# Kernel tuning notes

Hardware: AMD Instinct MI355X
Metric: run time of the kernel (lower is better)

Reference implementation:

```python
import jax, jax.numpy as jnp
import numpy as np

N_TOKEN = 64
H = 16
D = 1024
D_K = 64
D_V = 64
S3 = 30  # 3 * S, number of gated leading positions
GATE_INIT = 10.0


def setup_inputs() -> dict:
    key = jax.random.key(0)
    ks = jax.random.split(key, 8)
    B, L = 32, 2048
    x = jax.random.normal(ks[0], (B, L, D), dtype=jnp.float32)
    q_init = (1.0 / D_K) ** 0.5
    q_tok = jax.random.uniform(ks[1], (1, N_TOKEN, D), minval=-q_init, maxval=q_init, dtype=jnp.float32)
    scale = 0.02
    Wq = jax.random.normal(ks[2], (D, H * D_K), dtype=jnp.float32) * scale
    Wk = jax.random.normal(ks[3], (D, H * D_K), dtype=jnp.float32) * scale
    Wv = jax.random.normal(ks[4], (D, H * D_V), dtype=jnp.float32) * scale
    Wfc = jax.random.normal(ks[5], (H * D_V, D), dtype=jnp.float32) * scale
    gate_logit = -jnp.ones((S3,), dtype=jnp.float32) * GATE_INIT  # matches module init
    gamma = jnp.ones((D,), dtype=jnp.float32)
    beta = jnp.zeros((D,), dtype=jnp.float32)
    return {"x": x, "q_tok": q_tok, "Wq": Wq, "Wk": Wk, "Wv": Wv, "Wfc": Wfc,
            "gate_logit": gate_logit, "gamma": gamma, "beta": beta}


def reference(x, q_tok, Wq, Wk, Wv, Wfc, gate_logit, gamma, beta):
    # x: [B, L, D]; q_tok: [1, n_token, D]. Dropout is identity (eval mode).
    B, L, _ = x.shape
    temp = D_K ** 0.5

    # Cumulative-product gate over the first 30 positions (the torch for-loop).
    gate = jnp.cumprod(1.0 - jax.nn.sigmoid(gate_logit))  # [30]
    x1 = x.at[:, :S3].multiply(gate[None, :, None])

    q = (q_tok @ Wq).reshape(N_TOKEN, H, D_K)          # [n, H, dk]
    k = (x @ Wk).reshape(B, L, H, D_K)                  # [B, L, H, dk]
    v = (x1 @ Wv).reshape(B, L, H, D_V)                 # [B, L, H, dv]

    scores = jnp.einsum('nhd,blhd->bhnl', q / temp, k)  # [B, H, n, L]
    attn = jax.nn.softmax(scores, axis=-1)
    out = jnp.einsum('bhnl,blhd->bnhd', attn, v).reshape(B, N_TOKEN, H * D_V)

    out = out @ Wfc + q_tok                              # residual with query tokens

    # LayerNorm over last dim, eps=1e-6
    mu = jnp.mean(out, axis=-1, keepdims=True)
    var = jnp.mean(jnp.square(out - mu), axis=-1, keepdims=True)
    out = (out - mu) * jax.lax.rsqrt(var + 1e-6) * gamma + beta
    return out
```

## Files before the change

kernel.cpp:

```cpp
#include <hip/hip_runtime.h>
#include <stdint.h>

typedef unsigned short u16;
typedef short bf16x8 __attribute__((ext_vector_type(8)));
typedef float f32x4 __attribute__((ext_vector_type(4)));

__device__ __forceinline__ u16 f2b(float f) {
  uint32_t u = __builtin_bit_cast(uint32_t, f);
  u += 0x7fffu + ((u >> 16) & 1u);
  return (u16)(u >> 16);
}

__device__ __forceinline__ void gload_lds16(const void* g, void* l) {
  __builtin_amdgcn_global_load_lds(
      (const __attribute__((address_space(1))) void*)g,
      (__attribute__((address_space(3))) void*)l, 16, 0, 0);
}

__global__ void gate_kernel(const float* __restrict__ gl, float* __restrict__ gate) {
  if (threadIdx.x == 0 && blockIdx.x == 0) {
    float g = 1.0f;
    for (int i = 0; i < 30; ++i) {
      float s = 1.0f / (1.0f + __expf(-gl[i]));
      g *= (1.0f - s);
      gate[i] = g;
    }
  }
}

__global__ __launch_bounds__(256) void cvt_x_kernel(const float* __restrict__ x,
                                                    u16* __restrict__ xb) {
  int64_t i = ((int64_t)blockIdx.x * 256 + threadIdx.x) * 8;
  float4 a = *(const float4*)(x + i);
  float4 b = *(const float4*)(x + i + 4);
  union { u16 u[8]; bf16x8 v; } o;
  o.u[0] = f2b(a.x); o.u[1] = f2b(a.y); o.u[2] = f2b(a.z); o.u[3] = f2b(a.w);
  o.u[4] = f2b(b.x); o.u[5] = f2b(b.y); o.u[6] = f2b(b.z); o.u[7] = f2b(b.w);
  *(bf16x8*)(xb + i) = o.v;
}

__global__ __launch_bounds__(256) void transpose_w_kernel(const float* __restrict__ src,
                                                          u16* __restrict__ dst) {
  __shared__ float ls[64][65];
  int t = threadIdx.x;
  int bx = blockIdx.x & 15;
  int by = blockIdx.x >> 4;
  int r0 = by * 64, c0 = bx * 64;
  int tr = t >> 6, tc = t & 63;
#pragma unroll
  for (int i = 0; i < 16; ++i)
    ls[tr + i * 4][tc] = src[(int64_t)(r0 + tr + i * 4) * 1024 + c0 + tc];
  __syncthreads();
#pragma unroll
  for (int i = 0; i < 16; ++i)
    dst[(int64_t)(c0 + tr + i * 4) * 1024 + r0 + tc] = f2b(ls[tc][tr + i * 4]);
}

__global__ __launch_bounds__(256) void q_kernel(const float* __restrict__ q_tok,
                                                const float* __restrict__ Wq,
                                                u16* __restrict__ qb) {
  __shared__ float Qs[64][65];
  __shared__ float Ws[64][65];
  int h = blockIdx.x;
  int t = threadIdx.x;
  int tn = t >> 4, tk = t & 15;
  float acc[4][4] = {};
  for (int dt = 0; dt < 16; ++dt) {
    __syncthreads();
#pragma unroll
    for (int i = 0; i < 16; ++i) {
      int idx = t + i * 256;
      int rr = idx >> 6, cc = idx & 63;
      Qs[rr][cc] = q_tok[rr * 1024 + dt * 64 + cc];
      Ws[rr][cc] = Wq[(dt * 64 + rr) * 1024 + h * 64 + cc];
    }
    __syncthreads();
    for (int d = 0; d < 64; ++d) {
      float qv[4], wv[4];
#pragma unroll
      for (int i = 0; i < 4; ++i) qv[i] = Qs[tn * 4 + i][d];
#pragma unroll
      for (int j = 0; j < 4; ++j) wv[j] = Ws[d][tk * 4 + j];
#pragma unroll
      for (int i = 0; i < 4; ++i)
#pragma unroll
        for (int j = 0; j < 4; ++j) acc[i][j] += qv[i] * wv[j];
    }
  }
  const float sc = 1.44269504f / 8.0f;
#pragma unroll
  for (int i = 0; i < 4; ++i)
#pragma unroll
    for (int j = 0; j < 4; ++j)
      qb[(h * 64 + tn * 4 + i) * 64 + tk * 4 + j] = f2b(acc[i][j] * sc);
}

__global__ __launch_bounds__(256) void kv_gemm_kernel(
    const u16* __restrict__ xb, const u16* __restrict__ wkvT,
    const float* __restrict__ gate, u16* __restrict__ kbuf, u16* __restrict__ vT) {
  __shared__ u16 As[4096];
  __shared__ u16 Bs[4096];
  int bid = blockIdx.x;
  int mb = bid >> 4, nb = bid & 15;
  int m0 = mb * 128, n0 = nb * 128;
  int t = threadIdx.x, w = t >> 6, lane = t & 63;
  int wm = (w >> 1) * 64, wn = (w & 1) * 64;
  bool isV = (n0 >= 1024);
  f32x4 acc[4][4] = {};
  int srow = w * 32 + (lane >> 2);
  int scol = (lane & 3) * 8;
  const u16* aSrc = xb + (int64_t)(m0 + srow) * 1024 + scol;
  const u16* bSrc = wkvT + (int64_t)(n0 + srow) * 1024 + scol;
  u16* aDst = As + w * 1024;
  u16* bDst = Bs + w * 1024;
  for (int kt = 0; kt < 32; ++kt) {
    __syncthreads();
    int ko = kt * 32;
    gload_lds16(aSrc + ko, aDst);
    gload_lds16(aSrc + 16 * 1024 + ko, aDst + 512);
    gload_lds16(bSrc + ko, bDst);
    gload_lds16(bSrc + 16 * 1024 + ko, bDst + 512);
    __syncthreads();
    int l15 = lane & 15, lh = (lane >> 4) * 8;
    bf16x8 af[4], bf[4];
#pragma unroll
    for (int i = 0; i < 4; ++i) af[i] = *(const bf16x8*)(As + (wm + i * 16 + l15) * 32 + lh);
#pragma unroll
    for (int j = 0; j < 4; ++j) bf[j] = *(const bf16x8*)(Bs + (wn + j * 16 + l15) * 32 + lh);
    if (!isV) {
#pragma unroll
      for (int i = 0; i < 4; ++i)
#pragma unroll
        for (int j = 0; j < 4; ++j)
          acc[i][j] = __builtin_amdgcn_mfma_f32_16x16x32_bf16(af[i], bf[j], acc[i][j], 0, 0, 0);
    } else {
#pragma unroll
      for (int i = 0; i < 4; ++i)
#pragma unroll
        for (int j = 0; j < 4; ++j)
          acc[i][j] = __builtin_amdgcn_mfma_f32_16x16x32_bf16(bf[i], af[j], acc[i][j], 0, 0, 0);
    }
  }
  int b = m0 >> 11, lbase = m0 & 2047;
  int l15 = lane & 15, lr = (lane >> 4) * 4;
  if (!isV) {
#pragma unroll
    for (int i = 0; i < 4; ++i)
#pragma unroll
      for (int j = 0; j < 4; ++j) {
        int gcol = n0 + wn + j * 16 + l15;
        int h = gcol >> 6, dk = gcol & 63;
#pragma unroll
        for (int r = 0; r < 4; ++r) {
          int l = lbase + wm + i * 16 + lr + r;
          kbuf[(int64_t)((b * 16 + h) * 2048 + l) * 64 + dk] = f2b(acc[i][j][r]);
        }
      }
  } else {
#pragma unroll
    for (int j = 0; j < 4; ++j) {
      int lloc = wm + j * 16 + l15;
      int l = lbase + lloc;
      float g = 1.0f;
      if (lbase == 0 && lloc < 30) g = gate[lloc];
#pragma unroll
      for (int i = 0; i < 4; ++i) {
#pragma unroll
        for (int r = 0; r < 4; ++r) {
          int gn = (n0 - 1024) + wn + i * 16 + lr + r;
          int h = gn >> 6, dv = gn & 63;
          vT[(int64_t)((b * 16 + h) * 64 + dv) * 2048 + l] = f2b(acc[i][j][r] * g);
        }
      }
    }
  }
}

__global__ __launch_bounds__(256) void attn_kernel(
    const u16* __restrict__ qb, const u16* __restrict__ kbuf,
    const u16* __restrict__ vT, u16* __restrict__ attnout) {
  __shared__ u16 Ps[4096];
  int bid = blockIdx.x;
  int b = bid >> 4, h = bid & 15;
  int t = threadIdx.x, w = t >> 6, lane = t & 63;
  int l15 = lane & 15, lh8 = (lane >> 4) * 8;
  bf16x8 qf0 = *(const bf16x8*)(qb + (h * 64 + w * 16 + l15) * 64 + lh8);
  bf16x8 qf1 = *(const bf16x8*)(qb + (h * 64 + w * 16 + l15) * 64 + 32 + lh8);
  const u16* kB = kbuf + (int64_t)(b * 16 + h) * (2048 * 64);
  const u16* vB = vT + (int64_t)(b * 16 + h) * (64 * 2048);
  char* PsW = (char*)Ps + w * 2048;
  float m_r[4] = {-1e30f, -1e30f, -1e30f, -1e30f};
  float s_r[4] = {0.f, 0.f, 0.f, 0.f};
  f32x4 O[4] = {};
  for (int lt = 0; lt < 32; ++lt) {
    int l0 = lt * 64;
    f32x4 S[4];
#pragma unroll
    for (int ls = 0; ls < 4; ++ls) {
      const u16* kr = kB + (l0 + ls * 16 + l15) * 64 + lh8;
      bf16x8 k0 = *(const bf16x8*)(kr);
      bf16x8 k1 = *(const bf16x8*)(kr + 32);
      f32x4 s = {};
      s = __builtin_amdgcn_mfma_f32_16x16x32_bf16(qf0, k0, s, 0, 0, 0);
      s = __builtin_amdgcn_mfma_f32_16x16x32_bf16(qf1, k1, s, 0, 0, 0);
      S[ls] = s;
    }
    float scale[4];
#pragma unroll
    for (int r = 0; r < 4; ++r) {
      float tm = fmaxf(fmaxf(S[0][r], S[1][r]), fmaxf(S[2][r], S[3][r]));
#pragma unroll
      for (int msk = 1; msk < 16; msk <<= 1)
        tm = fmaxf(tm, __shfl_xor(tm, msk, 16));
      float mn = fmaxf(m_r[r], tm);
      scale[r] = exp2f(m_r[r] - mn);
      m_r[r] = mn;
    }
#pragma unroll
    for (int ls = 0; ls < 4; ++ls)
#pragma unroll
      for (int r = 0; r < 4; ++r) S[ls][r] = exp2f(S[ls][r] - m_r[r]);
#pragma unroll
    for (int r = 0; r < 4; ++r) {
      float ps = (S[0][r] + S[1][r]) + (S[2][r] + S[3][r]);
      s_r[r] = s_r[r] * scale[r] + ps;
    }
#pragma unroll
    for (int ls = 0; ls < 4; ++ls)
#pragma unroll
      for (int r = 0; r < 4; ++r) {
        int row = (lane >> 4) * 4 + r;
        int off = (ls * 16 + l15) * 2;
        *(u16*)(PsW + row * 128 + (off ^ ((row & 7) << 4))) = f2b(S[ls][r]);
      }
#pragma unroll
    for (int d = 0; d < 4; ++d)
#pragma unroll
      for (int r = 0; r < 4; ++r) O[d][r] *= scale[r];
    bf16x8 pa0, pa1;
    {
      int off0 = (lane >> 4) * 16;
      pa0 = *(const bf16x8*)(PsW + l15 * 128 + (off0 ^ ((l15 & 7) << 4)));
      pa1 = *(const bf16x8*)(PsW + l15 * 128 + ((off0 + 64) ^ ((l15 & 7) << 4)));
    }
#pragma unroll
    for (int d = 0; d < 4; ++d) {
      const u16* vr = vB + (d * 16 + l15) * 2048 + l0 + lh8;
      bf16x8 v0 = *(const bf16x8*)(vr);
      bf16x8 v1 = *(const bf16x8*)(vr + 32);
      O[d] = __builtin_amdgcn_mfma_f32_16x16x32_bf16(pa0, v0, O[d], 0, 0, 0);
      O[d] = __builtin_amdgcn_mfma_f32_16x16x32_bf16(pa1, v1, O[d], 0, 0, 0);
    }
  }
#pragma unroll
  for (int r = 0; r < 4; ++r) {
    float s = s_r[r];
#pragma unroll
    for (int msk = 1; msk < 16; msk <<= 1) s += __shfl_xor(s, msk, 16);
    float inv = 1.0f / s;
#pragma unroll
    for (int d = 0; d < 4; ++d) O[d][r] *= inv;
  }
#pragma unroll
  for (int d = 0; d < 4; ++d)
#pragma unroll
    for (int r = 0; r < 4; ++r) {
      int n = w * 16 + (lane >> 4) * 4 + r;
      attnout[(int64_t)(b * 64 + n) * 1024 + h * 64 + d * 16 + l15] = f2b(O[d][r]);
    }
}

__global__ __launch_bounds__(256) void fc_gemm_kernel(
    const u16* __restrict__ a, const u16* __restrict__ bT,
    const float* __restrict__ q_tok, float* __restrict__ out) {
  __shared__ u16 As[4096];
  __shared__ u16 Bs[4096];
  int bid = blockIdx.x;
  int mb = bid >> 3, nb = bid & 7;
  int m0 = mb * 128, n0 = nb * 128;
  int t = threadIdx.x, w = t >> 6, lane = t & 63;
  int wm = (w >> 1) * 64, wn = (w & 1) * 64;
  f32x4 acc[4][4] = {};
  int srow = w * 32 + (lane >> 2);
  int scol = (lane & 3) * 8;
  const u16* aSrc = a + (int64_t)(m0 + srow) * 1024 + scol;
  const u16* bSrc = bT + (int64_t)(n0 + srow) * 1024 + scol;
  u16* aDst = As + w * 1024;
  u16* bDst = Bs + w * 1024;
  for (int kt = 0; kt < 32; ++kt) {
    __syncthreads();
    int ko = kt * 32;
    gload_lds16(aSrc + ko, aDst);
    gload_lds16(aSrc + 16 * 1024 + ko, aDst + 512);
    gload_lds16(bSrc + ko, bDst);
    gload_lds16(bSrc + 16 * 1024 + ko, bDst + 512);
    __syncthreads();
    int l15 = lane & 15, lh = (lane >> 4) * 8;
    bf16x8 af[4], bf[4];
#pragma unroll
    for (int i = 0; i < 4; ++i) af[i] = *(const bf16x8*)(As + (wm + i * 16 + l15) * 32 + lh);
#pragma unroll
    for (int j = 0; j < 4; ++j) bf[j] = *(const bf16x8*)(Bs + (wn + j * 16 + l15) * 32 + lh);
#pragma unroll
    for (int i = 0; i < 4; ++i)
#pragma unroll
      for (int j = 0; j < 4; ++j)
        acc[i][j] = __builtin_amdgcn_mfma_f32_16x16x32_bf16(af[i], bf[j], acc[i][j], 0, 0, 0);
  }
  int l15 = lane & 15, lr = (lane >> 4) * 4;
#pragma unroll
  for (int i = 0; i < 4; ++i)
#pragma unroll
    for (int j = 0; j < 4; ++j) {
      int col = n0 + wn + j * 16 + l15;
#pragma unroll
      for (int r = 0; r < 4; ++r) {
        int row = m0 + wm + i * 16 + lr + r;
        out[(int64_t)row * 1024 + col] = acc[i][j][r] + q_tok[(row & 63) * 1024 + col];
      }
    }
}

__global__ __launch_bounds__(256) void ln_kernel(
    const float* __restrict__ fc, const float* __restrict__ gamma,
    const float* __restrict__ beta, float* __restrict__ out) {
  __shared__ float red[8];
  int row = blockIdx.x, t = threadIdx.x;
  float4 y = *(const float4*)(fc + (int64_t)row * 1024 + t * 4);
  float s = (y.x + y.y) + (y.z + y.w);
  float ss = (y.x * y.x + y.y * y.y) + (y.z * y.z + y.w * y.w);
#pragma unroll
  for (int msk = 1; msk < 64; msk <<= 1) {
    s += __shfl_xor(s, msk, 64);
    ss += __shfl_xor(ss, msk, 64);
  }
  if ((t & 63) == 0) { red[t >> 6] = s; red[4 + (t >> 6)] = ss; }
  __syncthreads();
  s = (red[0] + red[1]) + (red[2] + red[3]);
  ss = (red[4] + red[5]) + (red[6] + red[7]);
  float mu = s * (1.0f / 1024.0f);
  float var = ss * (1.0f / 1024.0f) - mu * mu;
  float rstd = rsqrtf(var + 1e-6f);
  float4 g = *(const float4*)(gamma + t * 4);
  float4 be = *(const float4*)(beta + t * 4);
  float4 o;
  o.x = (y.x - mu) * rstd * g.x + be.x;
  o.y = (y.y - mu) * rstd * g.y + be.y;
  o.z = (y.z - mu) * rstd * g.z + be.z;
  o.w = (y.w - mu) * rstd * g.w + be.w;
  *(float4*)(out + (int64_t)row * 1024 + t * 4) = o;
}

extern "C" void kernel_launch(void* const* d_in, const int* in_sizes, int n_in,
                              void* d_out, int out_size, void* d_ws, size_t ws_size,
                              hipStream_t stream) {
  const float* x     = (const float*)d_in[0];
  const float* q_tok = (const float*)d_in[1];
  const float* Wq    = (const float*)d_in[2];
  const float* Wk    = (const float*)d_in[3];
  const float* Wv    = (const float*)d_in[4];
  const float* Wfc   = (const float*)d_in[5];
  const float* gl    = (const float*)d_in[6];
  const float* gamma = (const float*)d_in[7];
  const float* beta  = (const float*)d_in[8];
  float* out = (float*)d_out;
  char* ws = (char*)d_ws;

  u16*   xb      = (u16*)(ws);
  u16*   kbuf    = (u16*)(ws + 134217728);
  u16*   vT      = (u16*)(ws + 268435456);
  u16*   wkvT    = (u16*)(ws + 402653184);
  u16*   wfcT    = (u16*)(ws + 406847488);
  u16*   qb      = (u16*)(ws + 408944640);
  float* gate    = (float*)(ws + 409075712);
  u16*   attnout = (u16*)(ws + 409076224);
  float* fcout   = (float*)(ws + 413270528);

  gate_kernel<<<1, 64, 0, stream>>>(gl, gate);
  cvt_x_kernel<<<32768, 256, 0, stream>>>(x, xb);
  transpose_w_kernel<<<256, 256, 0, stream>>>(Wk, wkvT);
  transpose_w_kernel<<<256, 256, 0, stream>>>(Wv, wkvT + 1024 * 1024);
  transpose_w_kernel<<<256, 256, 0, stream>>>(Wfc, wfcT);
  q_kernel<<<16, 256, 0, stream>>>(q_tok, Wq, qb);
  kv_gemm_kernel<<<8192, 256, 0, stream>>>(xb, wkvT, gate, kbuf, vT);
  attn_kernel<<<512, 256, 0, stream>>>(qb, kbuf, vT, attnout);
  fc_gemm_kernel<<<128, 256, 0, stream>>>(attnout, wfcT, q_tok, fcout);
  ln_kernel<<<2048, 256, 0, stream>>>(fcout, gamma, beta, out);
}
```

Before: 800.4 us.

## Rework GEMMs with swizzled K=64 LDS tiles, split-K attention, and MFMA q projection

The KV, FC and new Q GEMMs load 64-wide K tiles into XOR-swizzled LDS, which halves the number of barriers and avoids bank conflicts. Epilogues write vectorised 64-bit and float4 stores, and the KV GEMM block order is remapped for L2 locality. Attention is split four ways along L into 2048 blocks and followed by a separate combine kernel, which raises occupancy. The q projection becomes a bf16 MFMA GEMM. In exchange this adds extra launches and partial-result traffic, and the partials reuse the xb workspace region after it is consumed.

```diff
diff --git a/kernel.cpp b/kernel.cpp
--- a/kernel.cpp
+++ b/kernel.cpp
@@ -28,15 +28,15 @@
   }
 }
 
-__global__ __launch_bounds__(256) void cvt_x_kernel(const float* __restrict__ x,
-                                                    u16* __restrict__ xb) {
+__global__ __launch_bounds__(256) void cvt_kernel(const float* __restrict__ src,
+                                                  u16* __restrict__ dst) {
   int64_t i = ((int64_t)blockIdx.x * 256 + threadIdx.x) * 8;
-  float4 a = *(const float4*)(x + i);
-  float4 b = *(const float4*)(x + i + 4);
+  float4 a = *(const float4*)(src + i);
+  float4 b = *(const float4*)(src + i + 4);
   union { u16 u[8]; bf16x8 v; } o;
   o.u[0] = f2b(a.x); o.u[1] = f2b(a.y); o.u[2] = f2b(a.z); o.u[3] = f2b(a.w);
   o.u[4] = f2b(b.x); o.u[5] = f2b(b.y); o.u[6] = f2b(b.z); o.u[7] = f2b(b.w);
-  *(bf16x8*)(xb + i) = o.v;
+  *(bf16x8*)(dst + i) = o.v;
 }
 
 __global__ __launch_bounds__(256) void transpose_w_kernel(const float* __restrict__ src,
@@ -56,121 +56,145 @@
     dst[(int64_t)(c0 + tr + i * 4) * 1024 + r0 + tc] = f2b(ls[tc][tr + i * 4]);
 }
 
-__global__ __launch_bounds__(256) void q_kernel(const float* __restrict__ q_tok,
-                                                const float* __restrict__ Wq,
-                                                u16* __restrict__ qb) {
-  __shared__ float Qs[64][65];
-  __shared__ float Ws[64][65];
-  int h = blockIdx.x;
-  int t = threadIdx.x;
-  int tn = t >> 4, tk = t & 15;
-  float acc[4][4] = {};
-  for (int dt = 0; dt < 16; ++dt) {
-    __syncthreads();
-#pragma unroll
-    for (int i = 0; i < 16; ++i) {
-      int idx = t + i * 256;
-      int rr = idx >> 6, cc = idx & 63;
-      Qs[rr][cc] = q_tok[rr * 1024 + dt * 64 + cc];
-      Ws[rr][cc] = Wq[(dt * 64 + rr) * 1024 + h * 64 + cc];
-    }
-    __syncthreads();
-    for (int d = 0; d < 64; ++d) {
-      float qv[4], wv[4];
-#pragma unroll
-      for (int i = 0; i < 4; ++i) qv[i] = Qs[tn * 4 + i][d];
-#pragma unroll
-      for (int j = 0; j < 4; ++j) wv[j] = Ws[d][tk * 4 + j];
-#pragma unroll
-      for (int i = 0; i < 4; ++i)
-#pragma unroll
-        for (int j = 0; j < 4; ++j) acc[i][j] += qv[i] * wv[j];
+__global__ __launch_bounds__(256, 4) void q_gemm_kernel(
+    const u16* __restrict__ qtokb, const u16* __restrict__ wqT, u16* __restrict__ qb) {
+  __shared__ u16 As[4096];
+  __shared__ u16 Bs[8192];
+  int n0 = blockIdx.x * 128;
+  int t = threadIdx.x, w = t >> 6, lane = t & 63;
+  int wn = w * 32;
+  f32x4 acc[2][4] = {};
+  int l3 = lane >> 3;
+  int colE = ((lane & 7) ^ l3) * 8;
+  const u16* aS = qtokb + (int64_t)(w * 16 + l3) * 1024 + colE;
+  const u16* bS = wqT + (int64_t)(n0 + w * 32 + l3) * 1024 + colE;
+  u16* aD = As + w * 1024;
+  u16* bD = Bs + w * 2048;
+  int l15 = lane & 15, g16 = lane >> 4;
+  for (int kt = 0; kt < 16; ++kt) {
+    int ko = kt * 64;
+    __syncthreads();
+    gload_lds16(aS + ko, aD);
+    gload_lds16(aS + ko + 8192, aD + 512);
+#pragma unroll
+    for (int g = 0; g < 4; ++g) gload_lds16(bS + ko + g * 8192, bD + g * 512);
+    __syncthreads();
+#pragma unroll
+    for (int kk = 0; kk < 2; ++kk) {
+      int sl = ((kk * 4 + g16) ^ (l15 & 7)) * 8;
+      bf16x8 af[4], bf[2];
+#pragma unroll
+      for (int j = 0; j < 4; ++j) af[j] = *(const bf16x8*)(As + (j * 16 + l15) * 64 + sl);
+#pragma unroll
+      for (int i = 0; i < 2; ++i) bf[i] = *(const bf16x8*)(Bs + (wn + i * 16 + l15) * 64 + sl);
+#pragma unroll
+      for (int i = 0; i < 2; ++i)
+#pragma unroll
+        for (int j = 0; j < 4; ++j)
+          acc[i][j] = __builtin_amdgcn_mfma_f32_16x16x32_bf16(bf[i], af[j], acc[i][j], 0, 0, 0);
     }
   }
   const float sc = 1.44269504f / 8.0f;
-#pragma unroll
-  for (int i = 0; i < 4; ++i)
-#pragma unroll
-    for (int j = 0; j < 4; ++j)
-      qb[(h * 64 + tn * 4 + i) * 64 + tk * 4 + j] = f2b(acc[i][j] * sc);
-}
-
-__global__ __launch_bounds__(256) void kv_gemm_kernel(
+  int lr = g16 * 4;
+#pragma unroll
+  for (int i = 0; i < 2; ++i) {
+    int colg = n0 + wn + i * 16 + lr;
+#pragma unroll
+    for (int j = 0; j < 4; ++j) {
+      int qrow = j * 16 + l15;
+      u16 p[4];
+#pragma unroll
+      for (int r = 0; r < 4; ++r) p[r] = f2b(acc[i][j][r] * sc);
+      *(uint64_t*)(qb + qrow * 1024 + colg) = *(uint64_t*)p;
+    }
+  }
+}
+
+__global__ __launch_bounds__(256, 4) void kv_gemm_kernel(
     const u16* __restrict__ xb, const u16* __restrict__ wkvT,
     const float* __restrict__ gate, u16* __restrict__ kbuf, u16* __restrict__ vT) {
-  __shared__ u16 As[4096];
-  __shared__ u16 Bs[4096];
-  int bid = blockIdx.x;
+  __shared__ u16 As[8192];
+  __shared__ u16 Bs[8192];
+  int bid0 = blockIdx.x;
+  int bid = (bid0 & 7) * 1024 + (bid0 >> 3);
   int mb = bid >> 4, nb = bid & 15;
   int m0 = mb * 128, n0 = nb * 128;
   int t = threadIdx.x, w = t >> 6, lane = t & 63;
   int wm = (w >> 1) * 64, wn = (w & 1) * 64;
   bool isV = (n0 >= 1024);
   f32x4 acc[4][4] = {};
-  int srow = w * 32 + (lane >> 2);
-  int scol = (lane & 3) * 8;
-  const u16* aSrc = xb + (int64_t)(m0 + srow) * 1024 + scol;
-  const u16* bSrc = wkvT + (int64_t)(n0 + srow) * 1024 + scol;
-  u16* aDst = As + w * 1024;
-  u16* bDst = Bs + w * 1024;
-  for (int kt = 0; kt < 32; ++kt) {
-    __syncthreads();
-    int ko = kt * 32;
-    gload_lds16(aSrc + ko, aDst);
-    gload_lds16(aSrc + 16 * 1024 + ko, aDst + 512);
-    gload_lds16(bSrc + ko, bDst);
-    gload_lds16(bSrc + 16 * 1024 + ko, bDst + 512);
-    __syncthreads();
-    int l15 = lane & 15, lh = (lane >> 4) * 8;
-    bf16x8 af[4], bf[4];
-#pragma unroll
-    for (int i = 0; i < 4; ++i) af[i] = *(const bf16x8*)(As + (wm + i * 16 + l15) * 32 + lh);
-#pragma unroll
-    for (int j = 0; j < 4; ++j) bf[j] = *(const bf16x8*)(Bs + (wn + j * 16 + l15) * 32 + lh);
-    if (!isV) {
-#pragma unroll
-      for (int i = 0; i < 4; ++i)
-#pragma unroll
-        for (int j = 0; j < 4; ++j)
-          acc[i][j] = __builtin_amdgcn_mfma_f32_16x16x32_bf16(af[i], bf[j], acc[i][j], 0, 0, 0);
-    } else {
-#pragma unroll
-      for (int i = 0; i < 4; ++i)
-#pragma unroll
-        for (int j = 0; j < 4; ++j)
-          acc[i][j] = __builtin_amdgcn_mfma_f32_16x16x32_bf16(bf[i], af[j], acc[i][j], 0, 0, 0);
+  int l3 = lane >> 3;
+  int colE = ((lane & 7) ^ l3) * 8;
+  const u16* aS = xb + (int64_t)(m0 + w * 32 + l3) * 1024 + colE;
+  const u16* bS = wkvT + (int64_t)(n0 + w * 32 + l3) * 1024 + colE;
+  u16* aD = As + w * 2048;
+  u16* bD = Bs + w * 2048;
+  int l15 = lane & 15, g16 = lane >> 4;
+  for (int kt = 0; kt < 16; ++kt) {
+    int ko = kt * 64;
+    __syncthreads();
+#pragma unroll
+    for (int g = 0; g < 4; ++g) {
+      gload_lds16(aS + ko + g * 8192, aD + g * 512);
+      gload_lds16(bS + ko + g * 8192, bD + g * 512);
+    }
+    __syncthreads();
+#pragma unroll
+    for (int kk = 0; kk < 2; ++kk) {
+      int sl = ((kk * 4 + g16) ^ (l15 & 7)) * 8;
+      bf16x8 af[4], bf[4];
+#pragma unroll
+      for (int i = 0; i < 4; ++i) af[i] = *(const bf16x8*)(As + (wm + i * 16 + l15) * 64 + sl);
+#pragma unroll
+      for (int j = 0; j < 4; ++j) bf[j] = *(const bf16x8*)(Bs + (wn + j * 16 + l15) * 64 + sl);
+      if (!isV) {
+#pragma unroll
+        for (int i = 0; i < 4; ++i)
+#pragma unroll
+          for (int j = 0; j < 4; ++j)
+            acc[i][j] = __builtin_amdgcn_mfma_f32_16x16x32_bf16(bf[i], af[j], acc[i][j], 0, 0, 0);
+      } else {
+#pragma unroll
+        for (int i = 0; i < 4; ++i)
+#pragma unroll
+          for (int j = 0; j < 4; ++j)
+            acc[i][j] = __builtin_amdgcn_mfma_f32_16x16x32_bf16(af[i], bf[j], acc[i][j], 0, 0, 0);
+      }
     }
   }
   int b = m0 >> 11, lbase = m0 & 2047;
-  int l15 = lane & 15, lr = (lane >> 4) * 4;
+  int lr = g16 * 4;
   if (!isV) {
 #pragma unroll
-    for (int i = 0; i < 4; ++i)
+    for (int i = 0; i < 4; ++i) {
+      int dkg = n0 + wn + i * 16 + lr;
+      int h = dkg >> 6, dkk = dkg & 63;
 #pragma unroll
       for (int j = 0; j < 4; ++j) {
-        int gcol = n0 + wn + j * 16 + l15;
-        int h = gcol >> 6, dk = gcol & 63;
+        int l = lbase + wm + j * 16 + l15;
+        u16 p[4];
+#pragma unroll
+        for (int r = 0; r < 4; ++r) p[r] = f2b(acc[i][j][r]);
+        *(uint64_t*)(kbuf + ((int64_t)((b * 16 + h) * 2048 + l)) * 64 + dkk) = *(uint64_t*)p;
+      }
+    }
+  } else {
+#pragma unroll
+    for (int j = 0; j < 4; ++j) {
+      int dvg = (n0 - 1024) + wn + j * 16 + l15;
+      int h = dvg >> 6, dv = dvg & 63;
+#pragma unroll
+      for (int i = 0; i < 4; ++i) {
+        int lg = lbase + wm + i * 16 + lr;
+        u16 p[4];
 #pragma unroll
         for (int r = 0; r < 4; ++r) {
-          int l = lbase + wm + i * 16 + lr + r;
-          kbuf[(int64_t)((b * 16 + h) * 2048 + l) * 64 + dk] = f2b(acc[i][j][r]);
+          float val = acc[i][j][r];
+          int ll = lg + r;
+          if (ll < 30) val *= gate[ll];
+          p[r] = f2b(val);
         }
-      }
-  } else {
-#pragma unroll
-    for (int j = 0; j < 4; ++j) {
-      int lloc = wm + j * 16 + l15;
-      int l = lbase + lloc;
-      float g = 1.0f;
-      if (lbase == 0 && lloc < 30) g = gate[lloc];
-#pragma unroll
-      for (int i = 0; i < 4; ++i) {
-#pragma unroll
-        for (int r = 0; r < 4; ++r) {
-          int gn = (n0 - 1024) + wn + i * 16 + lr + r;
-          int h = gn >> 6, dv = gn & 63;
-          vT[(int64_t)((b * 16 + h) * 64 + dv) * 2048 + l] = f2b(acc[i][j][r] * g);
-        }
+        *(uint64_t*)(vT + ((int64_t)((b * 16 + h) * 64 + dv)) * 2048 + lg) = *(uint64_t*)p;
       }
     }
   }
@@ -178,22 +202,23 @@
 
 __global__ __launch_bounds__(256) void attn_kernel(
     const u16* __restrict__ qb, const u16* __restrict__ kbuf,
-    const u16* __restrict__ vT, u16* __restrict__ attnout) {
+    const u16* __restrict__ vT, float* __restrict__ pO,
+    float* __restrict__ pm, float* __restrict__ ps) {
   __shared__ u16 Ps[4096];
   int bid = blockIdx.x;
-  int b = bid >> 4, h = bid & 15;
+  int b = bid >> 6, h = (bid >> 2) & 15, c = bid & 3;
   int t = threadIdx.x, w = t >> 6, lane = t & 63;
-  int l15 = lane & 15, lh8 = (lane >> 4) * 8;
-  bf16x8 qf0 = *(const bf16x8*)(qb + (h * 64 + w * 16 + l15) * 64 + lh8);
-  bf16x8 qf1 = *(const bf16x8*)(qb + (h * 64 + w * 16 + l15) * 64 + 32 + lh8);
+  int l15 = lane & 15, g16 = lane >> 4, lh8 = g16 * 8;
+  bf16x8 qf0 = *(const bf16x8*)(qb + (w * 16 + l15) * 1024 + h * 64 + lh8);
+  bf16x8 qf1 = *(const bf16x8*)(qb + (w * 16 + l15) * 1024 + h * 64 + 32 + lh8);
   const u16* kB = kbuf + (int64_t)(b * 16 + h) * (2048 * 64);
   const u16* vB = vT + (int64_t)(b * 16 + h) * (64 * 2048);
   char* PsW = (char*)Ps + w * 2048;
   float m_r[4] = {-1e30f, -1e30f, -1e30f, -1e30f};
   float s_r[4] = {0.f, 0.f, 0.f, 0.f};
   f32x4 O[4] = {};
-  for (int lt = 0; lt < 32; ++lt) {
-    int l0 = lt * 64;
+  for (int lt = 0; lt < 8; ++lt) {
+    int l0 = c * 512 + lt * 64;
     f32x4 S[4];
 #pragma unroll
     for (int ls = 0; ls < 4; ++ls) {
@@ -222,14 +247,14 @@
       for (int r = 0; r < 4; ++r) S[ls][r] = exp2f(S[ls][r] - m_r[r]);
 #pragma unroll
     for (int r = 0; r < 4; ++r) {
-      float ps = (S[0][r] + S[1][r]) + (S[2][r] + S[3][r]);
-      s_r[r] = s_r[r] * scale[r] + ps;
+      float psm = (S[0][r] + S[1][r]) + (S[2][r] + S[3][r]);
+      s_r[r] = s_r[r] * scale[r] + psm;
     }
 #pragma unroll
     for (int ls = 0; ls < 4; ++ls)
 #pragma unroll
       for (int r = 0; r < 4; ++r) {
-        int row = (lane >> 4) * 4 + r;
+        int row = g16 * 4 + r;
         int off = (ls * 16 + l15) * 2;
         *(u16*)(PsW + row * 128 + (off ^ ((row & 7) << 4))) = f2b(S[ls][r]);
       }
@@ -239,7 +264,7 @@
       for (int r = 0; r < 4; ++r) O[d][r] *= scale[r];
     bf16x8 pa0, pa1;
     {
-      int off0 = (lane >> 4) * 16;
+      int off0 = g16 * 16;
       pa0 = *(const bf16x8*)(PsW + l15 * 128 + (off0 ^ ((l15 & 7) << 4)));
       pa1 = *(const bf16x8*)(PsW + l15 * 128 + ((off0 + 64) ^ ((l15 & 7) << 4)));
     }
@@ -257,68 +282,106 @@
     float s = s_r[r];
 #pragma unroll
     for (int msk = 1; msk < 16; msk <<= 1) s += __shfl_xor(s, msk, 16);
-    float inv = 1.0f / s;
-#pragma unroll
-    for (int d = 0; d < 4; ++d) O[d][r] *= inv;
-  }
+    s_r[r] = s;
+  }
+  int64_t pbase = (int64_t)bid * 4096;
 #pragma unroll
   for (int d = 0; d < 4; ++d)
 #pragma unroll
     for (int r = 0; r < 4; ++r) {
-      int n = w * 16 + (lane >> 4) * 4 + r;
-      attnout[(int64_t)(b * 64 + n) * 1024 + h * 64 + d * 16 + l15] = f2b(O[d][r]);
-    }
-}
-
-__global__ __launch_bounds__(256) void fc_gemm_kernel(
+      int n = w * 16 + g16 * 4 + r;
+      pO[pbase + n * 64 + d * 16 + l15] = O[d][r];
+    }
+  if (l15 == 0) {
+#pragma unroll
+    for (int r = 0; r < 4; ++r) {
+      int n = w * 16 + g16 * 4 + r;
+      pm[bid * 64 + n] = m_r[r];
+      ps[bid * 64 + n] = s_r[r];
+    }
+  }
+}
+
+__global__ __launch_bounds__(256) void attn_combine_kernel(
+    const float* __restrict__ pO, const float* __restrict__ pm,
+    const float* __restrict__ ps, u16* __restrict__ attnout) {
+  int bh = blockIdx.x;
+  int b = bh >> 4, h = bh & 15;
+  int t = threadIdx.x;
+  int dv = t & 63, grp = t >> 6;
+#pragma unroll
+  for (int i = 0; i < 16; ++i) {
+    int n = grp * 16 + i;
+    int base = bh * 256 + n;
+    float m0 = pm[base], m1 = pm[base + 64], m2 = pm[base + 128], m3 = pm[base + 192];
+    float M = fmaxf(fmaxf(m0, m1), fmaxf(m2, m3));
+    float w0 = exp2f(m0 - M), w1 = exp2f(m1 - M), w2 = exp2f(m2 - M), w3 = exp2f(m3 - M);
+    float stot = w0 * ps[base] + w1 * ps[base + 64] + w2 * ps[base + 128] + w3 * ps[base + 192];
+    float inv = 1.0f / stot;
+    int64_t ob = (int64_t)bh * 16384 + n * 64 + dv;
+    float o = w0 * pO[ob] + w1 * pO[ob + 4096] + w2 * pO[ob + 8192] + w3 * pO[ob + 12288];
+    attnout[((int64_t)(b * 64 + n)) * 1024 + h * 64 + dv] = f2b(o * inv);
+  }
+}
+
+__global__ __launch_bounds__(256, 4) void fc_gemm_kernel(
     const u16* __restrict__ a, const u16* __restrict__ bT,
     const float* __restrict__ q_tok, float* __restrict__ out) {
-  __shared__ u16 As[4096];
-  __shared__ u16 Bs[4096];
+  __shared__ u16 As[8192];
+  __shared__ u16 Bs[8192];
   int bid = blockIdx.x;
   int mb = bid >> 3, nb = bid & 7;
   int m0 = mb * 128, n0 = nb * 128;
   int t = threadIdx.x, w = t >> 6, lane = t & 63;
   int wm = (w >> 1) * 64, wn = (w & 1) * 64;
   f32x4 acc[4][4] = {};
-  int srow = w * 32 + (lane >> 2);
-  int scol = (lane & 3) * 8;
-  const u16* aSrc = a + (int64_t)(m0 + srow) * 1024 + scol;
-  const u16* bSrc = bT + (int64_t)(n0 + srow) * 1024 + scol;
-  u16* aDst = As + w * 1024;
-  u16* bDst = Bs + w * 1024;
-  for (int kt = 0; kt < 32; ++kt) {
-    __syncthreads();
-    int ko = kt * 32;
-    gload_lds16(aSrc + ko, aDst);
-    gload_lds16(aSrc + 16 * 1024 + ko, aDst + 512);
-    gload_lds16(bSrc + ko, bDst);
-    gload_lds16(bSrc + 16 * 1024 + ko, bDst + 512);
-    __syncthreads();
-    int l15 = lane & 15, lh = (lane >> 4) * 8;
-    bf16x8 af[4], bf[4];
-#pragma unroll
-    for (int i = 0; i < 4; ++i) af[i] = *(const bf16x8*)(As + (wm + i * 16 + l15) * 32 + lh);
-#pragma unroll
-    for (int j = 0; j < 4; ++j) bf[j] = *(const bf16x8*)(Bs + (wn + j * 16 + l15) * 32 + lh);
-#pragma unroll
-    for (int i = 0; i < 4; ++i)
-#pragma unroll
-      for (int j = 0; j < 4; ++j)
-        acc[i][j] = __builtin_amdgcn_mfma_f32_16x16x32_bf16(af[i], bf[j], acc[i][j], 0, 0, 0);
-  }
-  int l15 = lane & 15, lr = (lane >> 4) * 4;
-#pragma unroll
-  for (int i = 0; i < 4; ++i)
+  int l3 = lane >> 3;
+  int colE = ((lane & 7) ^ l3) * 8;
+  const u16* aS = a + (int64_t)(m0 + w * 32 + l3) * 1024 + colE;
+  const u16* bS = bT + (int64_t)(n0 + w * 32 + l3) * 1024 + colE;
+  u16* aD = As + w * 2048;
+  u16* bD = Bs + w * 2048;
+  int l15 = lane & 15, g16 = lane >> 4;
+  for (int kt = 0; kt < 16; ++kt) {
+    int ko = kt * 64;
+    __syncthreads();
+#pragma unroll
+    for (int g = 0; g < 4; ++g) {
+      gload_lds16(aS + ko + g * 8192, aD + g * 512);
+      gload_lds16(bS + ko + g * 8192, bD + g * 512);
+    }
+    __syncthreads();
+#pragma unroll
+    for (int kk = 0; kk < 2; ++kk) {
+      int sl = ((kk * 4 + g16) ^ (l15 & 7)) * 8;
+      bf16x8 af[4], bf[4];
+#pragma unroll
+      for (int i = 0; i < 4; ++i) af[i] = *(const bf16x8*)(As + (wm + i * 16 + l15) * 64 + sl);
+#pragma unroll
+      for (int j = 0; j < 4; ++j) bf[j] = *(const bf16x8*)(Bs + (wn + j * 16 + l15) * 64 + sl);
+#pragma unroll
+      for (int i = 0; i < 4; ++i)
+#pragma unroll
+        for (int j = 0; j < 4; ++j)
+          acc[i][j] = __builtin_amdgcn_mfma_f32_16x16x32_bf16(bf[i], af[j], acc[i][j], 0, 0, 0);
+    }
+  }
+  int lr = g16 * 4;
+#pragma unroll
+  for (int i = 0; i < 4; ++i) {
+    int colg = n0 + wn + i * 16 + lr;
 #pragma unroll
     for (int j = 0; j < 4; ++j) {
-      int col = n0 + wn + j * 16 + l15;
-#pragma unroll
-      for (int r = 0; r < 4; ++r) {
-        int row = m0 + wm + i * 16 + lr + r;
-        out[(int64_t)row * 1024 + col] = acc[i][j][r] + q_tok[(row & 63) * 1024 + col];
-      }
-    }
+      int row = m0 + wm + j * 16 + l15;
+      float4 res = *(const float4*)(q_tok + (row & 63) * 1024 + colg);
+      float4 o;
+      o.x = acc[i][j][0] + res.x;
+      o.y = acc[i][j][1] + res.y;
+      o.z = acc[i][j][2] + res.z;
+      o.w = acc[i][j][3] + res.w;
+      *(float4*)(out + (int64_t)row * 1024 + colg) = o;
+    }
+  }
 }
 
 __global__ __launch_bounds__(256) void ln_kernel(
@@ -371,19 +434,27 @@
   u16*   vT      = (u16*)(ws + 268435456);
   u16*   wkvT    = (u16*)(ws + 402653184);
   u16*   wfcT    = (u16*)(ws + 406847488);
-  u16*   qb      = (u16*)(ws + 408944640);
-  float* gate    = (float*)(ws + 409075712);
-  u16*   attnout = (u16*)(ws + 409076224);
-  float* fcout   = (float*)(ws + 413270528);
+  u16*   wqT     = (u16*)(ws + 408944640);
+  u16*   qtokb   = (u16*)(ws + 411041792);
+  u16*   qb      = (u16*)(ws + 411172864);
+  float* gate    = (float*)(ws + 411303936);
+  u16*   attnout = (u16*)(ws + 411304448);
+  float* fcout   = (float*)(ws + 415498752);
+  float* pO = (float*)(ws);
+  float* pm = (float*)(ws + 33554432);
+  float* ps = (float*)(ws + 34078720);
 
   gate_kernel<<<1, 64, 0, stream>>>(gl, gate);
-  cvt_x_kernel<<<32768, 256, 0, stream>>>(x, xb);
+  cvt_kernel<<<32768, 256, 0, stream>>>(x, xb);
+  cvt_kernel<<<32, 256, 0, stream>>>(q_tok, qtokb);
   transpose_w_kernel<<<256, 256, 0, stream>>>(Wk, wkvT);
   transpose_w_kernel<<<256, 256, 0, stream>>>(Wv, wkvT + 1024 * 1024);
   transpose_w_kernel<<<256, 256, 0, stream>>>(Wfc, wfcT);
-  q_kernel<<<16, 256, 0, stream>>>(q_tok, Wq, qb);
+  transpose_w_kernel<<<256, 256, 0, stream>>>(Wq, wqT);
+  q_gemm_kernel<<<8, 256, 0, stream>>>(qtokb, wqT, qb);
   kv_gemm_kernel<<<8192, 256, 0, stream>>>(xb, wkvT, gate, kbuf, vT);
-  attn_kernel<<<512, 256, 0, stream>>>(qb, kbuf, vT, attnout);
+  attn_kernel<<<2048, 256, 0, stream>>>(qb, kbuf, vT, pO, pm, ps);
+  attn_combine_kernel<<<512, 256, 0, stream>>>(pO, pm, ps, attnout);
   fc_gemm_kernel<<<128, 256, 0, stream>>>(attnout, wfcT, q_tok, fcout);
   ln_kernel<<<2048, 256, 0, stream>>>(fcout, gamma, beta, out);
 }
```

After: 2.466 ms. +208.1%, slower.
